# Optimization experiments

Measured on AMD Instinct MI355X. Metric: run time of the kernel, lower is better.

The kernel has to match this reference:

```python
import jax, jax.numpy as jnp
import numpy as np

N = 50000      # nodes
E = 800000     # edges
IN = 128       # in_channels
H = 128        # hidden_channels
OUT = 500      # out_channels
EPS = 1e-5


def setup_inputs() -> dict:
    key = jax.random.key(0)
    ks = jax.random.split(key, 8)
    def rn(k, shape, scale=0.05):
        return jax.random.normal(k, shape, jnp.float32) * scale
    return {
        "x": jax.random.normal(ks[0], (N, IN), jnp.float32),
        "edge_index": jax.random.randint(ks[1], (2, E), 0, N, dtype=jnp.int32),
        "W1": rn(ks[2], (IN, H)), "b1": jnp.zeros((H,), jnp.float32),
        "g1": jnp.ones((H,), jnp.float32), "be1": jnp.zeros((H,), jnp.float32),
        "W2": rn(ks[3], (H, 2 * H)), "b2": jnp.zeros((2 * H,), jnp.float32),
        "g2": jnp.ones((2 * H,), jnp.float32), "be2": jnp.zeros((2 * H,), jnp.float32),
        "W3": rn(ks[4], (2 * H, H)), "b3": jnp.zeros((H,), jnp.float32),
        "g3": jnp.ones((H,), jnp.float32), "be3": jnp.zeros((H,), jnp.float32),
        "Wl1": rn(ks[5], (H, H // 2)), "bl1": jnp.zeros((H // 2,), jnp.float32),
        "g4": jnp.ones((H // 2,), jnp.float32), "be4": jnp.zeros((H // 2,), jnp.float32),
        "Wl2": rn(ks[6], (H // 2, OUT)), "bl2": jnp.zeros((OUT,), jnp.float32),
    }


def layer_norm(x, g, b):
    mu = jnp.mean(x, axis=-1, keepdims=True)
    var = jnp.mean(jnp.square(x - mu), axis=-1, keepdims=True)
    return (x - mu) * jax.lax.rsqrt(var + EPS) * g + b


def gcn_conv(x, W, b, src, dst, n):
    # PyG GCNConv: x' = D^{-1/2} (A + I) D^{-1/2} (x W) + b, with self-loops.
    h = x @ W                                   # [N, F]
    ones = jnp.ones(src.shape[0], h.dtype)
    deg = jax.ops.segment_sum(ones, dst, num_segments=n) + 1.0  # +1 self-loop
    dinv = jnp.where(deg > 0, jax.lax.rsqrt(deg), 0.0)          # [N]
    coef = dinv[src] * dinv[dst]                # [E]
    agg = jax.ops.segment_sum(h[src] * coef[:, None], dst, num_segments=n)
    agg = agg + h * jnp.square(dinv)[:, None]   # self-loop messages
    return agg + b


def reference(x, edge_index, W1, b1, g1, be1, W2, b2, g2, be2,
              W3, b3, g3, be3, Wl1, bl1, g4, be4, Wl2, bl2):
    # eval mode: dropout is identity
    src, dst = edge_index[0], edge_index[1]
    n = x.shape[0]
    h = jax.nn.elu(layer_norm(gcn_conv(x, W1, b1, src, dst, n), g1, be1))
    h = jax.nn.elu(layer_norm(gcn_conv(h, W2, b2, src, dst, n), g2, be2))
    h = jax.nn.elu(layer_norm(gcn_conv(h, W3, b3, src, dst, n), g3, be3))
    h = jax.nn.elu(layer_norm(h @ Wl1 + bl1, g4, be4))
    return h @ Wl2 + bl2
```

## Files before the change

kernel.cpp:

```cpp
#include <hip/hip_runtime.h>
#include <cstdint>


#define LN_EPS 1e-5f

typedef __attribute__((ext_vector_type(8))) short bf16x8;
typedef __attribute__((ext_vector_type(4))) float f32x4;

static __device__ __forceinline__ ushort f2bf(float f) {
  union { float f; uint u; } c; c.f = f;
  uint u = c.u;
  return (ushort)((u + 0x7fffu + ((u >> 16) & 1u)) >> 16);
}
static __device__ __forceinline__ float bf2f(ushort h) {
  union { uint u; float f; } c; c.u = (uint)h << 16;
  return c.f;
}


__global__ void deg_kernel(const int* __restrict__ dst, int* __restrict__ deg, int E) {
  int e = blockIdx.x * blockDim.x + threadIdx.x;
  if (e < E) atomicAdd(&deg[dst[e]], 1);
}

__global__ void scan1_kernel(const int* __restrict__ deg, int* __restrict__ excl,
                             int* __restrict__ bsums, float* __restrict__ dinv, int N) {
  __shared__ int s[256];
  int tid = threadIdx.x;
  int i = blockIdx.x * 256 + tid;
  int v = (i < N) ? deg[i] : 0;
  s[tid] = v;
  __syncthreads();
  for (int o = 1; o < 256; o <<= 1) {
    int t = (tid >= o) ? s[tid - o] : 0;
    __syncthreads();
    if (tid >= o) s[tid] += t;
    __syncthreads();
  }
  if (i < N) {
    excl[i] = s[tid] - v;
    dinv[i] = rsqrtf((float)v + 1.0f);
  }
  if (tid == 255) bsums[blockIdx.x] = s[tid];
}

__global__ void scan23_kernel(int* __restrict__ rowptr, int* __restrict__ fill,
                              const int* __restrict__ bsums, int N, int Etotal, int nb) {
  __shared__ int sh[256];
  const int tid = threadIdx.x;
  const int bix = blockIdx.x;
  int v = (tid < bix && tid < nb) ? bsums[tid] : 0;
  sh[tid] = v;
  __syncthreads();
  for (int o = 128; o > 0; o >>= 1) {
    if (tid < o) sh[tid] += sh[tid + o];
    __syncthreads();
  }
  const int off = sh[0];
  int i = bix * 256 + tid;
  if (i < N) {
    int r = rowptr[i] + off;
    rowptr[i] = r;
    fill[i] = r;
  } else if (i == N) {
    rowptr[N] = Etotal;
  }
}

__global__ void fill_kernel(const int* __restrict__ src, const int* __restrict__ dst,
                            int* __restrict__ fill, int* __restrict__ srcs, int E) {
  int e = blockIdx.x * blockDim.x + threadIdx.x;
  if (e >= E) return;
  int idx = atomicAdd(&fill[dst[e]], 1);
  srcs[idx] = src[e];
}


struct WConvArgs {
  const float* w[5];
  ushort* wt[5];
  int K[5], N[5];
  int off[6];
};

__global__ void prep_kernel(WConvArgs a, int total, int* __restrict__ deg, int Nn) {
  int i = blockIdx.x * blockDim.x + threadIdx.x;
  if (i < Nn) deg[i] = 0;
  if (i < 768) a.wt[4][32000 + i] = 0;
  if (i >= total) return;
  int m = 0;
  while (i >= a.off[m + 1]) m++;
  int j = i - a.off[m];
  int k = j / a.N[m], n = j - k * a.N[m];
  a.wt[m][(size_t)n * a.K[m] + k] = f2bf(a.w[m][j]);
}

#define TBM 128
#define TBN 128
#define TBK 32
#define LDK 40

template <int AF32>
__global__ __launch_bounds__(256, 2) void mfma_gemm_kernel(
    const void* __restrict__ A, const ushort* __restrict__ Bt,
    const float* __restrict__ bias, ushort* __restrict__ Cout,
    int M, int N, int K) {
  __shared__ ushort As[TBM][LDK];
  __shared__ ushort Bs[TBN][LDK];
  const int tid = threadIdx.x;
  const int lane = tid & 63;
  const int w = tid >> 6;
  const int wm = w & 1, wn = w >> 1;
  const int quad = lane >> 4, l16 = lane & 15;
  const int rowBase = blockIdx.y * TBM;
  const int colBase = blockIdx.x * TBN;

  f32x4 acc[4][4] = {};
  const int lr = tid >> 2;
  const int lk = (tid & 3) * 8;

  for (int k0 = 0; k0 < K; k0 += TBK) {
#pragma unroll
    for (int h = 0; h < 2; h++) {
      int r = lr + h * 64;
      int grow = rowBase + r;
      if (AF32) {
        const float* Af = (const float*)A;
        float4 v0 = make_float4(0.f, 0.f, 0.f, 0.f), v1 = v0;
        if (grow < M) {
          const float* ap = Af + (size_t)grow * K + k0 + lk;
          v0 = *(const float4*)ap;
          v1 = *(const float4*)(ap + 4);
        }
        uint4 wv;
        wv.x = (uint)f2bf(v0.x) | ((uint)f2bf(v0.y) << 16);
        wv.y = (uint)f2bf(v0.z) | ((uint)f2bf(v0.w) << 16);
        wv.z = (uint)f2bf(v1.x) | ((uint)f2bf(v1.y) << 16);
        wv.w = (uint)f2bf(v1.z) | ((uint)f2bf(v1.w) << 16);
        *(uint4*)&As[r][lk] = wv;
      } else {
        const ushort* Ab = (const ushort*)A;
        uint4 va = make_uint4(0, 0, 0, 0);
        if (grow < M) va = *(const uint4*)(Ab + (size_t)grow * K + k0 + lk);
        *(uint4*)&As[r][lk] = va;
      }
      int gcol = colBase + r;
      uint4 vb = make_uint4(0, 0, 0, 0);
      if (gcol < N) vb = *(const uint4*)(Bt + (size_t)gcol * K + k0 + lk);
      *(uint4*)&Bs[r][lk] = vb;
    }
    __syncthreads();
    bf16x8 af[4], bfr[4];
#pragma unroll
    for (int i = 0; i < 4; i++) {
      af[i]  = *(const bf16x8*)&As[wm * 64 + i * 16 + l16][quad * 8];
      bfr[i] = *(const bf16x8*)&Bs[wn * 64 + i * 16 + l16][quad * 8];
    }
#pragma unroll
    for (int i = 0; i < 4; i++)
#pragma unroll
      for (int j = 0; j < 4; j++)
        acc[i][j] = __builtin_amdgcn_mfma_f32_16x16x32_bf16(af[i], bfr[j], acc[i][j], 0, 0, 0);
    __syncthreads();
  }
#pragma unroll
  for (int i = 0; i < 4; i++) {
    int row0 = rowBase + wm * 64 + i * 16 + quad * 4;
#pragma unroll
    for (int j = 0; j < 4; j++) {
      int col = colBase + wn * 64 + j * 16 + l16;
      if (col >= N) continue;
      float bv = bias ? bias[col] : 0.f;
#pragma unroll
      for (int r = 0; r < 4; r++) {
        int row = row0 + r;
        if (row >= M) continue;
        Cout[(size_t)row * N + col] = f2bf(acc[i][j][r] + bv);
      }
    }
  }
}

__global__ __launch_bounds__(256, 2) void l45_kernel(
    const ushort* __restrict__ A, const ushort* __restrict__ Bt1,
    const float* __restrict__ bias1, const float* __restrict__ gamma,
    const float* __restrict__ beta, const ushort* __restrict__ Bt2,
    const float* __restrict__ bias2, float* __restrict__ Cout, int M) {
  __shared__ ushort As[128][LDK];
  __shared__ ushort Bs[64][LDK];
  __shared__ ushort h4s[128][68];
  __shared__ __align__(16) float sout[16][500];
  const int tid = threadIdx.x;
  const int lane = tid & 63;
  const int w = tid >> 6;
  const int wm = w & 1, wn = w >> 1;
  const int quad = lane >> 4, l16 = lane & 15;
  const int rowBase = blockIdx.x * 128;

  f32x4 acc[4][4] = {};
  const int lr = tid >> 2;
  const int lk = (tid & 3) * 8;

  for (int k0 = 0; k0 < 128; k0 += TBK) {
#pragma unroll
    for (int h = 0; h < 2; h++) {
      int r = lr + h * 64;
      int grow = rowBase + r;
      uint4 va = make_uint4(0, 0, 0, 0);
      if (grow < M) va = *(const uint4*)(A + (size_t)grow * 128 + k0 + lk);
      *(uint4*)&As[r][lk] = va;
      if (h == 0) {
        uint4 vb = *(const uint4*)(Bt1 + (size_t)r * 128 + k0 + lk);
        *(uint4*)&Bs[r][lk] = vb;
      }
    }
    __syncthreads();
    if (wn == 0) {
      bf16x8 af[4], bfr[4];
#pragma unroll
      for (int i = 0; i < 4; i++) {
        af[i]  = *(const bf16x8*)&As[wm * 64 + i * 16 + l16][quad * 8];
        bfr[i] = *(const bf16x8*)&Bs[i * 16 + l16][quad * 8];
      }
#pragma unroll
      for (int i = 0; i < 4; i++)
#pragma unroll
        for (int j = 0; j < 4; j++)
          acc[i][j] = __builtin_amdgcn_mfma_f32_16x16x32_bf16(af[i], bfr[j], acc[i][j], 0, 0, 0);
    }
    __syncthreads();
  }

  if (wn == 0) {
    const int rowB = wm * 64;
#pragma unroll
    for (int i = 0; i < 4; i++) {
#pragma unroll
      for (int r = 0; r < 4; r++) {
        int row = rowB + i * 16 + quad * 4 + r;
        float v[4];
        float s = 0.f;
#pragma unroll
        for (int j = 0; j < 4; j++) {
          v[j] = acc[i][j][r] + bias1[j * 16 + l16];
          s += v[j];
        }
#pragma unroll
        for (int o = 8; o >= 1; o >>= 1) s += __shfl_xor(s, o, 16);
        float mean = s * (1.0f / 64.0f);
        float q = 0.f;
#pragma unroll
        for (int j = 0; j < 4; j++) {
          float d = v[j] - mean;
          q += d * d;
        }
#pragma unroll
        for (int o = 8; o >= 1; o >>= 1) q += __shfl_xor(q, o, 16);
        float rstd = rsqrtf(q * (1.0f / 64.0f) + LN_EPS);
#pragma unroll
        for (int j = 0; j < 4; j++) {
          int col = j * 16 + l16;
          float y = (v[j] - mean) * rstd * gamma[col] + beta[col];
          y = (y > 0.f) ? y : expm1f(y);
          h4s[row][col] = f2bf(y);
        }
      }
    }
  }
  __syncthreads();

  bf16x8 breg[8][2];
  float bvreg[8];
#pragma unroll
  for (int c = 0; c < 8; c++) {
    const int bcol = (w * 8 + c) * 16 + l16;
    breg[c][0] = *(const bf16x8*)(Bt2 + (size_t)bcol * 64 + quad * 8);
    breg[c][1] = *(const bf16x8*)(Bt2 + (size_t)bcol * 64 + 32 + quad * 8);
    bvreg[c] = (bcol < 500) ? bias2[bcol] : 0.f;
  }

#pragma unroll 1
  for (int rt = 0; rt < 8; rt++) {
    bf16x8 a0 = *(const bf16x8*)&h4s[rt * 16 + l16][quad * 8];
    bf16x8 a1 = *(const bf16x8*)&h4s[rt * 16 + l16][quad * 8 + 32];
#pragma unroll
    for (int c = 0; c < 8; c++) {
      f32x4 pacc = {0.f, 0.f, 0.f, 0.f};
      pacc = __builtin_amdgcn_mfma_f32_16x16x32_bf16(a0, breg[c][0], pacc, 0, 0, 0);
      pacc = __builtin_amdgcn_mfma_f32_16x16x32_bf16(a1, breg[c][1], pacc, 0, 0, 0);
      const int col = (w * 8 + c) * 16 + l16;
      if (col < 500) {
#pragma unroll
        for (int r = 0; r < 4; r++)
          sout[quad * 4 + r][col] = pacc[r] + bvreg[c];
      }
    }
    __syncthreads();
#pragma unroll
    for (int k = 0; k < 8; k++) {
      int idx = k * 256 + tid;
      if (idx < 2000) {
        int r = idx / 125;
        int c4 = idx - r * 125;
        int grow = rowBase + rt * 16 + r;
        if (grow < M) {
          float4 v = *(float4*)&sout[r][c4 * 4];
          *(float4*)&Cout[(size_t)grow * 500 + c4 * 4] = v;
        }
      }
    }
    __syncthreads();
  }
}


static __device__ __forceinline__ void acc8(float* a, uint4 v, float c) {
  a[0] += c * bf2f((ushort)(v.x & 0xffffu)); a[1] += c * bf2f((ushort)(v.x >> 16));
  a[2] += c * bf2f((ushort)(v.y & 0xffffu)); a[3] += c * bf2f((ushort)(v.y >> 16));
  a[4] += c * bf2f((ushort)(v.z & 0xffffu)); a[5] += c * bf2f((ushort)(v.z >> 16));
  a[6] += c * bf2f((ushort)(v.w & 0xffffu)); a[7] += c * bf2f((ushort)(v.w >> 16));
}

__global__ __launch_bounds__(256) void agg_kernel(
    const ushort* __restrict__ hb, const int* __restrict__ rowptr,
    const int* __restrict__ srcs, const float* __restrict__ dinv,
    uint* __restrict__ out, int Nn) {
  const int wave = threadIdx.x >> 6;
  const int n = blockIdx.x * 4 + wave;
  if (n >= Nn) return;
  const int lane = threadIdx.x & 63;
  const int g = lane >> 4, l16 = lane & 15;
  const uint4* h4 = (const uint4*)hb;
  const float di = dinv[n];
  float a[8] = {0.f, 0.f, 0.f, 0.f, 0.f, 0.f, 0.f, 0.f};
  if (g == 0) {
    uint4 sv = h4[(size_t)n * 16 + l16];
    acc8(a, sv, di * di);
  }
  int i = rowptr[n] + g;
  const int e = rowptr[n + 1];
  for (; i + 4 < e; i += 8) {
    int s0 = srcs[i], s1 = srcs[i + 4];
    float c0 = dinv[s0] * di, c1 = dinv[s1] * di;
    uint4 v0 = h4[(size_t)s0 * 16 + l16];
    uint4 v1 = h4[(size_t)s1 * 16 + l16];
    acc8(a, v0, c0);
    acc8(a, v1, c1);
  }
  if (i < e) {
    int s = srcs[i];
    float c = dinv[s] * di;
    uint4 v = h4[(size_t)s * 16 + l16];
    acc8(a, v, c);
  }
#pragma unroll
  for (int k = 0; k < 8; k++) {
    a[k] += __shfl_xor(a[k], 16);
    a[k] += __shfl_xor(a[k], 32);
  }
  if (g == 0) {
    uint4 o;
    o.x = (uint)f2bf(a[0]) | ((uint)f2bf(a[1]) << 16);
    o.y = (uint)f2bf(a[2]) | ((uint)f2bf(a[3]) << 16);
    o.z = (uint)f2bf(a[4]) | ((uint)f2bf(a[5]) << 16);
    o.w = (uint)f2bf(a[6]) | ((uint)f2bf(a[7]) << 16);
    ((uint4*)out)[(size_t)n * 16 + l16] = o;
  }
}

__global__ __launch_bounds__(256) void agg_ln_kernel(
    const ushort* __restrict__ hb, const int* __restrict__ rowptr,
    const int* __restrict__ srcs, const float* __restrict__ dinv,
    const float* __restrict__ bias, const float* __restrict__ gamma,
    const float* __restrict__ beta, uint* __restrict__ out, int Nn) {
  const int wave = threadIdx.x >> 6;
  const int n = blockIdx.x * 4 + wave;
  if (n >= Nn) return;
  const int lane = threadIdx.x & 63;
  const int g = lane >> 4, l16 = lane & 15;
  const uint4* h4 = (const uint4*)hb;
  const float di = dinv[n];
  float a[8] = {0.f, 0.f, 0.f, 0.f, 0.f, 0.f, 0.f, 0.f};
  if (g == 0) {
    uint4 sv = h4[(size_t)n * 16 + l16];
    acc8(a, sv, di * di);
    float4 b0 = ((const float4*)bias)[l16 * 2];
    float4 b1 = ((const float4*)bias)[l16 * 2 + 1];
    a[0] += b0.x; a[1] += b0.y; a[2] += b0.z; a[3] += b0.w;
    a[4] += b1.x; a[5] += b1.y; a[6] += b1.z; a[7] += b1.w;
  }
  int i = rowptr[n] + g;
  const int e = rowptr[n + 1];
  for (; i + 4 < e; i += 8) {
    int s0 = srcs[i], s1 = srcs[i + 4];
    float c0 = dinv[s0] * di, c1 = dinv[s1] * di;
    uint4 v0 = h4[(size_t)s0 * 16 + l16];
    uint4 v1 = h4[(size_t)s1 * 16 + l16];
    acc8(a, v0, c0);
    acc8(a, v1, c1);
  }
  if (i < e) {
    int s = srcs[i];
    float c = dinv[s] * di;
    uint4 v = h4[(size_t)s * 16 + l16];
    acc8(a, v, c);
  }
#pragma unroll
  for (int k = 0; k < 8; k++) {
    a[k] += __shfl_xor(a[k], 16);
    a[k] += __shfl_xor(a[k], 32);
  }
  float s = ((a[0] + a[1]) + (a[2] + a[3])) + ((a[4] + a[5]) + (a[6] + a[7]));
  s += __shfl_xor(s, 8);
  s += __shfl_xor(s, 4);
  s += __shfl_xor(s, 2);
  s += __shfl_xor(s, 1);
  float mean = s * (1.0f / 128.0f);
  float q = 0.f;
#pragma unroll
  for (int k = 0; k < 8; k++) {
    float d = a[k] - mean;
    q += d * d;
  }
  q += __shfl_xor(q, 8);
  q += __shfl_xor(q, 4);
  q += __shfl_xor(q, 2);
  q += __shfl_xor(q, 1);
  float rstd = rsqrtf(q * (1.0f / 128.0f) + LN_EPS);
  if (g == 0) {
    float4 g0 = ((const float4*)gamma)[l16 * 2];
    float4 g1 = ((const float4*)gamma)[l16 * 2 + 1];
    float4 e0 = ((const float4*)beta)[l16 * 2];
    float4 e1 = ((const float4*)beta)[l16 * 2 + 1];
    float gv[8] = {g0.x, g0.y, g0.z, g0.w, g1.x, g1.y, g1.z, g1.w};
    float ev[8] = {e0.x, e0.y, e0.z, e0.w, e1.x, e1.y, e1.z, e1.w};
    float y[8];
#pragma unroll
    for (int k = 0; k < 8; k++) {
      float t = (a[k] - mean) * rstd * gv[k] + ev[k];
      y[k] = (t > 0.f) ? t : expm1f(t);
    }
    uint4 o;
    o.x = (uint)f2bf(y[0]) | ((uint)f2bf(y[1]) << 16);
    o.y = (uint)f2bf(y[2]) | ((uint)f2bf(y[3]) << 16);
    o.z = (uint)f2bf(y[4]) | ((uint)f2bf(y[5]) << 16);
    o.w = (uint)f2bf(y[6]) | ((uint)f2bf(y[7]) << 16);
    ((uint4*)out)[(size_t)n * 16 + l16] = o;
  }
}

template <int F, bool IN_BF16>
__global__ __launch_bounds__(F) void ln_elu_kernel(const void* __restrict__ xin,
                                                   const float* __restrict__ g,
                                                   const float* __restrict__ be,
                                                   ushort* __restrict__ out) {
  constexpr int NW = (F + 63) / 64;
  __shared__ float sb[NW];
  const int row = blockIdx.x;
  const int f = threadIdx.x;
  float v;
  if (IN_BF16) v = bf2f(((const ushort*)xin)[(size_t)row * F + f]);
  else         v = ((const float*)xin)[(size_t)row * F + f];
  float s = v;
#pragma unroll
  for (int o = 32; o >= 1; o >>= 1) s += __shfl_xor(s, o);
  float mean;
  if constexpr (NW == 1) {
    mean = s * (1.0f / F);
  } else {
    if ((f & 63) == 0) sb[f >> 6] = s;
    __syncthreads();
    float t = 0.f;
#pragma unroll
    for (int w2 = 0; w2 < NW; w2++) t += sb[w2];
    mean = t * (1.0f / F);
    __syncthreads();
  }
  float d = v - mean;
  float q = d * d;
#pragma unroll
  for (int o = 32; o >= 1; o >>= 1) q += __shfl_xor(q, o);
  float var;
  if constexpr (NW == 1) {
    var = q * (1.0f / F);
  } else {
    if ((f & 63) == 0) sb[f >> 6] = q;
    __syncthreads();
    float t = 0.f;
#pragma unroll
    for (int w2 = 0; w2 < NW; w2++) t += sb[w2];
    var = t * (1.0f / F);
  }
  float y = d * rsqrtf(var + LN_EPS) * g[f] + be[f];
  out[(size_t)row * F + f] = f2bf((y > 0.f) ? y : expm1f(y));
}


extern "C" void kernel_launch(void* const* d_in, const int* in_sizes, int n_in,
                              void* d_out, int out_size, void* d_ws, size_t ws_size,
                              hipStream_t stream) {
  const float* x   = (const float*)d_in[0];
  const int*   ei  = (const int*)d_in[1];
  const float* W1  = (const float*)d_in[2];
  const float* b1  = (const float*)d_in[3];
  const float* g1  = (const float*)d_in[4];
  const float* be1 = (const float*)d_in[5];
  const float* W2  = (const float*)d_in[6];
  const float* b2  = (const float*)d_in[7];
  const float* g2  = (const float*)d_in[8];
  const float* be2 = (const float*)d_in[9];
  const float* W3  = (const float*)d_in[10];
  const float* b3  = (const float*)d_in[11];
  const float* g3  = (const float*)d_in[12];
  const float* be3 = (const float*)d_in[13];
  const float* Wl1 = (const float*)d_in[14];
  const float* bl1 = (const float*)d_in[15];
  const float* g4  = (const float*)d_in[16];
  const float* be4 = (const float*)d_in[17];
  const float* Wl2 = (const float*)d_in[18];
  const float* bl2 = (const float*)d_in[19];

  const int N = in_sizes[0] / 128;
  const int E = in_sizes[1] / 2;
  const int* esrc = ei;
  const int* edst = ei + E;

  char* p = (char*)d_ws;
  ushort* Pb = (ushort*)p;            p += (size_t)N * 256 * 2;
  ushort* Qb = (ushort*)p;            p += (size_t)N * 256 * 2;
  ushort* W1t = (ushort*)p;           p += 128 * 128 * 2;
  ushort* W2t = (ushort*)p;           p += 128 * 256 * 2;
  ushort* W3t = (ushort*)p;           p += 256 * 128 * 2;
  ushort* Wl1t = (ushort*)p;          p += 128 * 64 * 2;
  ushort* Wl2t = (ushort*)p;          p += 64 * 512 * 2;
  int*   srcs  = (int*)p;             p += (size_t)E * 4;
  int*   deg   = (int*)p;             p += (size_t)N * 4;
  float* dinv  = (float*)p;           p += (size_t)N * 4;
  int*   rowptr= (int*)p;             p += (size_t)(N + 2) * 4;
  int*   fill  = (int*)p;             p += (size_t)N * 4;
  int*   bsums = (int*)p;             p += 256 * 4;

  const int nb = (N + 255) / 256;
  const int eb = (E + 255) / 256;

  WConvArgs wa;
  wa.w[0] = W1;  wa.wt[0] = W1t;  wa.K[0] = 128; wa.N[0] = 128;
  wa.w[1] = W2;  wa.wt[1] = W2t;  wa.K[1] = 128; wa.N[1] = 256;
  wa.w[2] = W3;  wa.wt[2] = W3t;  wa.K[2] = 256; wa.N[2] = 128;
  wa.w[3] = Wl1; wa.wt[3] = Wl1t; wa.K[3] = 128; wa.N[3] = 64;
  wa.w[4] = Wl2; wa.wt[4] = Wl2t; wa.K[4] = 64;  wa.N[4] = 500;
  wa.off[0] = 0;
  for (int m = 0; m < 5; m++) wa.off[m + 1] = wa.off[m] + wa.K[m] * wa.N[m];
  int wtotal = wa.off[5];
  int ptotal = wtotal > N ? wtotal : N;
  prep_kernel<<<(ptotal + 255) / 256, 256, 0, stream>>>(wa, wtotal, deg, N);

  deg_kernel<<<eb, 256, 0, stream>>>(edst, deg, E);
  scan1_kernel<<<nb, 256, 0, stream>>>(deg, rowptr, bsums, dinv, N);
  scan23_kernel<<<(N + 256) / 256, 256, 0, stream>>>(rowptr, fill, bsums, N, E, nb);
  fill_kernel<<<eb, 256, 0, stream>>>(esrc, edst, fill, srcs, E);

  const int ab = (N + 3) / 4;
  auto grid_of = [&](int M, int Nn) {
    return dim3((Nn + TBN - 1) / TBN, (M + TBM - 1) / TBM);
  };

  mfma_gemm_kernel<1><<<grid_of(N, 128), 256, 0, stream>>>(
      x, W1t, nullptr, Pb, N, 128, 128);
  agg_ln_kernel<<<ab, 256, 0, stream>>>(Pb, rowptr, srcs, dinv, b1, g1, be1, (uint*)Qb, N);

  agg_kernel<<<ab, 256, 0, stream>>>(Qb, rowptr, srcs, dinv, (uint*)Pb, N);
  mfma_gemm_kernel<0><<<grid_of(N, 256), 256, 0, stream>>>(
      Pb, W2t, b2, Qb, N, 256, 128);
  ln_elu_kernel<256, true><<<N, 256, 0, stream>>>(Qb, g2, be2, Pb);

  mfma_gemm_kernel<0><<<grid_of(N, 128), 256, 0, stream>>>(
      Pb, W3t, nullptr, Qb, N, 128, 256);
  agg_ln_kernel<<<ab, 256, 0, stream>>>(Qb, rowptr, srcs, dinv, b3, g3, be3, (uint*)Pb, N);

  l45_kernel<<<dim3((N + 127) / 128), 256, 0, stream>>>(
      Pb, Wl1t, bl1, g4, be4, Wl2t, bl2, (float*)d_out, N);
}
```

Before: 496.6 us.

## Split fused final MLP kernel into separate layer-4 and layer-5 kernels

The fused l45 kernel is split in two. l4_kernel runs the 128->64 GEMM with LayerNorm and ELU and writes a bf16 intermediate to global memory. l5_kernel then runs the 64->500 projection with 16 rows per block, which gives far more blocks and lower LDS use per block (launch bound raised to 4). The serial 8-iteration row-tile loop and its syncs are gone, so the large 100MB fp32 output write is spread across many more workgroups. The cost is an extra kernel launch plus a small global round-trip of the intermediate, and Bt2 is reloaded per block.

```diff
diff --git a/kernel.cpp b/kernel.cpp
--- a/kernel.cpp
+++ b/kernel.cpp
@@ -181,15 +181,12 @@
   }
 }
 
-__global__ __launch_bounds__(256, 2) void l45_kernel(
+__global__ __launch_bounds__(256, 2) void l4_kernel(
     const ushort* __restrict__ A, const ushort* __restrict__ Bt1,
     const float* __restrict__ bias1, const float* __restrict__ gamma,
-    const float* __restrict__ beta, const ushort* __restrict__ Bt2,
-    const float* __restrict__ bias2, float* __restrict__ Cout, int M) {
+    const float* __restrict__ beta, ushort* __restrict__ Hout, int M) {
   __shared__ ushort As[128][LDK];
   __shared__ ushort Bs[64][LDK];
-  __shared__ ushort h4s[128][68];
-  __shared__ __align__(16) float sout[16][500];
   const int tid = threadIdx.x;
   const int lane = tid & 63;
   const int w = tid >> 6;
@@ -231,43 +228,64 @@
     __syncthreads();
   }
 
-  if (wn == 0) {
-    const int rowB = wm * 64;
-#pragma unroll
-    for (int i = 0; i < 4; i++) {
-#pragma unroll
-      for (int r = 0; r < 4; r++) {
-        int row = rowB + i * 16 + quad * 4 + r;
-        float v[4];
-        float s = 0.f;
-#pragma unroll
-        for (int j = 0; j < 4; j++) {
-          v[j] = acc[i][j][r] + bias1[j * 16 + l16];
-          s += v[j];
-        }
-#pragma unroll
-        for (int o = 8; o >= 1; o >>= 1) s += __shfl_xor(s, o, 16);
-        float mean = s * (1.0f / 64.0f);
-        float q = 0.f;
-#pragma unroll
-        for (int j = 0; j < 4; j++) {
-          float d = v[j] - mean;
-          q += d * d;
-        }
-#pragma unroll
-        for (int o = 8; o >= 1; o >>= 1) q += __shfl_xor(q, o, 16);
-        float rstd = rsqrtf(q * (1.0f / 64.0f) + LN_EPS);
+  if (wn != 0) return;
+  const int rowB = wm * 64;
+#pragma unroll
+  for (int i = 0; i < 4; i++) {
+#pragma unroll
+    for (int r = 0; r < 4; r++) {
+      int row = rowB + i * 16 + quad * 4 + r;
+      float v[4];
+      float s = 0.f;
+#pragma unroll
+      for (int j = 0; j < 4; j++) {
+        v[j] = acc[i][j][r] + bias1[j * 16 + l16];
+        s += v[j];
+      }
+#pragma unroll
+      for (int o = 8; o >= 1; o >>= 1) s += __shfl_xor(s, o, 16);
+      float mean = s * (1.0f / 64.0f);
+      float q = 0.f;
+#pragma unroll
+      for (int j = 0; j < 4; j++) {
+        float d = v[j] - mean;
+        q += d * d;
+      }
+#pragma unroll
+      for (int o = 8; o >= 1; o >>= 1) q += __shfl_xor(q, o, 16);
+      float rstd = rsqrtf(q * (1.0f / 64.0f) + LN_EPS);
+      int grow = rowBase + row;
+      if (grow < M) {
 #pragma unroll
         for (int j = 0; j < 4; j++) {
           int col = j * 16 + l16;
           float y = (v[j] - mean) * rstd * gamma[col] + beta[col];
           y = (y > 0.f) ? y : expm1f(y);
-          h4s[row][col] = f2bf(y);
+          Hout[(size_t)grow * 64 + col] = f2bf(y);
         }
       }
     }
   }
-  __syncthreads();
+}
+
+__global__ __launch_bounds__(256, 4) void l5_kernel(
+    const ushort* __restrict__ H, const ushort* __restrict__ Bt2,
+    const float* __restrict__ bias2, float* __restrict__ Cout, int M) {
+  __shared__ ushort h4s[16][68];
+  __shared__ __align__(16) float sout[16][500];
+  const int tid = threadIdx.x;
+  const int lane = tid & 63;
+  const int w = tid >> 6;
+  const int quad = lane >> 4, l16 = lane & 15;
+  const int rowBase = blockIdx.x * 16;
+
+  if (tid < 128) {
+    int r = tid >> 3, c8 = (tid & 7) * 8;
+    int grow = rowBase + r;
+    uint4 v = make_uint4(0, 0, 0, 0);
+    if (grow < M) v = *(const uint4*)(H + (size_t)grow * 64 + c8);
+    *(uint4*)&h4s[r][c8] = v;
+  }
 
   bf16x8 breg[8][2];
   float bvreg[8];
@@ -278,38 +296,36 @@
     breg[c][1] = *(const bf16x8*)(Bt2 + (size_t)bcol * 64 + 32 + quad * 8);
     bvreg[c] = (bcol < 500) ? bias2[bcol] : 0.f;
   }
-
-#pragma unroll 1
-  for (int rt = 0; rt < 8; rt++) {
-    bf16x8 a0 = *(const bf16x8*)&h4s[rt * 16 + l16][quad * 8];
-    bf16x8 a1 = *(const bf16x8*)&h4s[rt * 16 + l16][quad * 8 + 32];
-#pragma unroll
-    for (int c = 0; c < 8; c++) {
-      f32x4 pacc = {0.f, 0.f, 0.f, 0.f};
-      pacc = __builtin_amdgcn_mfma_f32_16x16x32_bf16(a0, breg[c][0], pacc, 0, 0, 0);
-      pacc = __builtin_amdgcn_mfma_f32_16x16x32_bf16(a1, breg[c][1], pacc, 0, 0, 0);
-      const int col = (w * 8 + c) * 16 + l16;
-      if (col < 500) {
-#pragma unroll
-        for (int r = 0; r < 4; r++)
-          sout[quad * 4 + r][col] = pacc[r] + bvreg[c];
-      }
-    }
-    __syncthreads();
-#pragma unroll
-    for (int k = 0; k < 8; k++) {
-      int idx = k * 256 + tid;
-      if (idx < 2000) {
-        int r = idx / 125;
-        int c4 = idx - r * 125;
-        int grow = rowBase + rt * 16 + r;
-        if (grow < M) {
-          float4 v = *(float4*)&sout[r][c4 * 4];
-          *(float4*)&Cout[(size_t)grow * 500 + c4 * 4] = v;
-        }
-      }
-    }
-    __syncthreads();
+  __syncthreads();
+
+  bf16x8 a0 = *(const bf16x8*)&h4s[l16][quad * 8];
+  bf16x8 a1 = *(const bf16x8*)&h4s[l16][quad * 8 + 32];
+#pragma unroll
+  for (int c = 0; c < 8; c++) {
+    f32x4 pacc = {0.f, 0.f, 0.f, 0.f};
+    pacc = __builtin_amdgcn_mfma_f32_16x16x32_bf16(a0, breg[c][0], pacc, 0, 0, 0);
+    pacc = __builtin_amdgcn_mfma_f32_16x16x32_bf16(a1, breg[c][1], pacc, 0, 0, 0);
+    const int col = (w * 8 + c) * 16 + l16;
+    if (col < 500) {
+#pragma unroll
+      for (int r = 0; r < 4; r++)
+        sout[quad * 4 + r][col] = pacc[r] + bvreg[c];
+    }
+  }
+  __syncthreads();
+
+#pragma unroll
+  for (int k = 0; k < 8; k++) {
+    int idx = k * 256 + tid;
+    if (idx < 2000) {
+      int r = idx / 125;
+      int c4 = idx - r * 125;
+      int grow = rowBase + r;
+      if (grow < M) {
+        float4 v = *(float4*)&sout[r][c4 * 4];
+        *(float4*)&Cout[(size_t)grow * 500 + c4 * 4] = v;
+      }
+    }
   }
 }
 
@@ -578,6 +594,9 @@
       Pb, W3t, nullptr, Qb, N, 128, 256);
   agg_ln_kernel<<<ab, 256, 0, stream>>>(Qb, rowptr, srcs, dinv, b3, g3, be3, (uint*)Pb, N);
 
-  l45_kernel<<<dim3((N + 127) / 128), 256, 0, stream>>>(
-      Pb, Wl1t, bl1, g4, be4, Wl2t, bl2, (float*)d_out, N);
-}
+  l4_kernel<<<dim3((N + 127) / 128), 256, 0, stream>>>(
+      Pb, Wl1t, bl1, g4, be4, Qb, N);
+
+  l5_kernel<<<dim3((N + 15) / 16), 256, 0, stream>>>(
+      Qb, Wl2t, bl2, (float*)d_out, N);
+}
```

After: 514.5 us. +3.6%, slower.
